# Performance work log

Hardware: AMD Instinct MI355X
Metric: run time of the kernel (lower is better)

The kernel has to match this reference:

```python
import jax, jax.numpy as jnp
import numpy as np

# dims matching init_kwargs
L = 2          # lstm_depth
H = 512        # lstm_size
E = 512        # text_embedding_size
V = 32000      # vocab_size
FH = 512       # feature_embedding_hidden_size
FEAT = 2048    # feature_size
START_IDX = 3.0  # start_of_seq_token_idx (used as a fill value, per original code)


def _lstm_cell(x, h, c, Wih, Whh, b):
    # PyTorch gate order: i, f, g, o. Wih:[in,4H], Whh:[H,4H], b:[4H]
    gates = x @ Wih + h @ Whh + b  # [B,4H]
    i, f, g, o = jnp.split(gates, 4, axis=-1)
    c_new = jax.nn.sigmoid(f) * c + jax.nn.sigmoid(i) * jnp.tanh(g)
    h_new = jax.nn.sigmoid(o) * jnp.tanh(c_new)
    return h_new, c_new


def setup_inputs() -> dict:
    key = jax.random.key(0)
    ks = jax.random.split(key, 12)
    B, N, T = 64, 49, 40
    s = 0.02
    img_data = jax.random.normal(ks[0], (B, N, FEAT), jnp.float32)
    W_fh = jax.random.normal(ks[1], (FEAT, FH), jnp.float32) * s
    b_fh = jnp.zeros((FH,), jnp.float32)
    Wc = jax.random.normal(ks[2], (L, FH, H), jnp.float32) * s
    bc = jnp.zeros((L, H), jnp.float32)
    Wh = jax.random.normal(ks[3], (L, FH, H), jnp.float32) * s
    bh = jnp.zeros((L, H), jnp.float32)
    W_ih = jax.random.normal(ks[4], (L, E, 4 * H), jnp.float32) * 0.04
    W_hh = jax.random.normal(ks[5], (L, H, 4 * H), jnp.float32) * 0.04
    b_lstm = jnp.zeros((L, 4 * H), jnp.float32)
    emb = jax.random.normal(ks[6], (V, E), jnp.float32) * s
    u = jax.random.uniform(ks[7], (T, B, V), jnp.float32, minval=1e-6, maxval=1.0 - 1e-6)
    gumbel = -jnp.log(-jnp.log(u))  # Gumbel(0,1) noise: Gumbel-max == Categorical.sample
    return {
        "img_data": img_data, "W_fh": W_fh, "b_fh": b_fh,
        "Wc": Wc, "bc": bc, "Wh": Wh, "bh": bh,
        "W_ih": W_ih, "W_hh": W_hh, "b_lstm": b_lstm,
        "emb": emb, "gumbel": gumbel, "max_seq_len": 40,
    }


def reference(img_data, W_fh, b_fh, Wc, bc, Wh, bh, W_ih, W_hh, b_lstm, emb, gumbel, max_seq_len):
    B = img_data.shape[0]
    # f_embedding = tanh(Linear(img_data)) : [B,N,FH]
    f_emb = jnp.tanh(img_data @ W_fh + b_fh)
    # mean over regions commutes with the per-layer Linear: mean(f @ W + b) = mean(f) @ W + b
    f_mean = jnp.mean(f_emb, axis=1)  # [B,FH]
    c0 = jnp.einsum('bf,lfh->lbh', f_mean, Wc) + bc[:, None, :]  # [L,B,H]
    h0 = jnp.einsum('bf,lfh->lbh', f_mean, Wh) + bh[:, None, :]
    # initial "embedding" is zeros + start_of_seq_token_idx (a constant fill, per original)
    x0 = jnp.full((B, E), START_IDX, dtype=img_data.dtype)
    emb_T = emb.T  # [E,V]

    def step(carry, g_t):
        h, c, x = carry  # h,c:[L,B,H], x:[B,E]; g_t:[B,V]
        inp = x
        hs, cs = [], []
        for l in range(L):  # small static depth
            hn, cn = _lstm_cell(inp, h[l], c[l], W_ih[l], W_hh[l], b_lstm[l])
            hs.append(hn); cs.append(cn)
            inp = hn
        logits = inp @ emb_T                      # [B,V]
        logp = jax.nn.log_softmax(logits, axis=-1)
        tok = jnp.argmax(logp + g_t, axis=-1)     # Gumbel-max categorical sample
        lp = jnp.take_along_axis(logp, tok[:, None], axis=1)[:, 0]  # [B]
        x_next = emb[tok]                         # next-step embedding lookup
        return (jnp.stack(hs, 0), jnp.stack(cs, 0), x_next), (tok, lp)

    _, (tokens, log_probs) = jax.lax.scan(step, (h0, c0, x0), gumbel)
    return tokens.T, log_probs.T  # [B,T], [B,T]
```

## Files before the change

kernel.cpp:

```cpp
#include <hip/hip_runtime.h>
#include <cmath>

namespace {

constexpr int BATCH = 64;
constexpr int NREG  = 49;
constexpr int FEATN = 2048;
constexpr int FHN   = 512;
constexpr int HID   = 512;
constexpr int EMBN  = 512;
constexpr int VOC   = 32000;
constexpr int TSTEPS= 40;
constexpr int G4    = 2048;
constexpr int NVT   = VOC / 128;

typedef short bf16x8 __attribute__((ext_vector_type(8)));
typedef float f32x4  __attribute__((ext_vector_type(4)));

__device__ __forceinline__ float sigm(float x) { return 1.0f / (1.0f + expf(-x)); }

__device__ __forceinline__ unsigned short f2bf(float f) {
  unsigned u = __float_as_uint(f);
  unsigned r = (u + 0x7fffu + ((u >> 16) & 1u)) >> 16;
  return (unsigned short)r;
}
__device__ __forceinline__ float bf2f(unsigned short h) {
  return __uint_as_float(((unsigned)h) << 16);
}

__device__ __forceinline__ bool better(float a, int ia, float b, int ib) {
  return a > b || (a == b && ia < ib);
}
__device__ __forceinline__ void top2_merge(float& v1, int& i1, float& v2, int& i2,
                                           float u1, int j1, float u2, int j2) {
  if (better(u1, j1, v1, i1)) {
    float t = v1; int ti = i1;
    v1 = u1; i1 = j1;
    if (better(u2, j2, t, ti)) { v2 = u2; i2 = j2; } else { v2 = t; i2 = ti; }
  } else {
    if (better(u1, j1, v2, i2)) { v2 = u1; i2 = j1; }
  }
}
__device__ __forceinline__ void lse_merge(float& m, float& s, float om, float os) {
  float nm = fmaxf(m, om);
  float ns = 0.f;
  if (m  > -INFINITY) ns += s  * expf(m  - nm);
  if (om > -INFINITY) ns += os * expf(om - nm);
  m = nm; s = ns;
}

__global__ __launch_bounds__(256) void k_trans(const float* __restrict__ src,
    unsigned short* __restrict__ dhi, unsigned short* __restrict__ dlo, int K, int N) {
  __shared__ float tile[32][33];
  const int k0 = blockIdx.x * 32, n0 = blockIdx.y * 32;
  const int tx = threadIdx.x & 31, ty = threadIdx.x >> 5;
#pragma unroll
  for (int r = ty; r < 32; r += 8) tile[r][tx] = src[(size_t)(k0 + r) * N + n0 + tx];
  __syncthreads();
#pragma unroll
  for (int r = ty; r < 32; r += 8) {
    float v = tile[tx][r];
    unsigned short hv = f2bf(v);
    size_t o = (size_t)(n0 + r) * K + k0 + tx;
    dhi[o] = hv;
    dlo[o] = f2bf(v - bf2f(hv));
  }
}

__global__ void k_split(const float* __restrict__ src, unsigned short* __restrict__ dhi,
                        unsigned short* __restrict__ dlo) {
  const size_t i = (size_t)blockIdx.x * 256 + threadIdx.x;
  const float4* p = reinterpret_cast<const float4*>(src) + i * 2;
  float4 a = p[0], b = p[1];
  float v[8] = {a.x, a.y, a.z, a.w, b.x, b.y, b.z, b.w};
  unsigned short hi[8], lo[8];
#pragma unroll
  for (int j = 0; j < 8; ++j) {
    hi[j] = f2bf(v[j]);
    lo[j] = f2bf(v[j] - bf2f(hi[j]));
  }
  uint4 oh, ol;
  oh.x = hi[0] | (hi[1] << 16); oh.y = hi[2] | (hi[3] << 16);
  oh.z = hi[4] | (hi[5] << 16); oh.w = hi[6] | (hi[7] << 16);
  ol.x = lo[0] | (lo[1] << 16); ol.y = lo[2] | (lo[3] << 16);
  ol.z = lo[4] | (lo[5] << 16); ol.w = lo[6] | (lo[7] << 16);
  reinterpret_cast<uint4*>(dhi)[i] = oh;
  reinterpret_cast<uint4*>(dlo)[i] = ol;
}

__global__ void k_emb2bf(const float* __restrict__ emb, unsigned short* __restrict__ ebf) {
  const size_t i = (size_t)blockIdx.x * 256 + threadIdx.x;
  const float4* p = reinterpret_cast<const float4*>(emb) + i * 2;
  float4 a = p[0], b = p[1];
  uint4 o;
  o.x = (unsigned)f2bf(a.x) | ((unsigned)f2bf(a.y) << 16);
  o.y = (unsigned)f2bf(a.z) | ((unsigned)f2bf(a.w) << 16);
  o.z = (unsigned)f2bf(b.x) | ((unsigned)f2bf(b.y) << 16);
  o.w = (unsigned)f2bf(b.z) | ((unsigned)f2bf(b.w) << 16);
  reinterpret_cast<uint4*>(ebf)[i] = o;
}

__global__ __launch_bounds__(256) void k_feat_mfma(
    const unsigned short* __restrict__ Ahi, const unsigned short* __restrict__ Alo,
    const unsigned short* __restrict__ Bhi, const unsigned short* __restrict__ Blo,
    const float* __restrict__ bias, float* __restrict__ femb) {
  const int m0 = blockIdx.x * 64, n0 = blockIdx.y * 64;
  const int tid = threadIdx.x, lane = tid & 63, w = tid >> 6;
  const int l15 = lane & 15, l4 = lane >> 4;
  f32x4 acc[4];
#pragma unroll
  for (int nt = 0; nt < 4; ++nt) acc[nt] = (f32x4){0.f, 0.f, 0.f, 0.f};
  const size_t arow = (size_t)(m0 + w * 16 + l15) * FEATN;
  for (int kk = 0; kk < FEATN / 32; ++kk) {
    const int k = kk * 32 + l4 * 8;
    bf16x8 a1 = *reinterpret_cast<const bf16x8*>(Ahi + arow + k);
    bf16x8 a2 = *reinterpret_cast<const bf16x8*>(Alo + arow + k);
#pragma unroll
    for (int nt = 0; nt < 4; ++nt) {
      const size_t brow = (size_t)(n0 + nt * 16 + l15) * FEATN + k;
      bf16x8 b1 = *reinterpret_cast<const bf16x8*>(Bhi + brow);
      bf16x8 b2 = *reinterpret_cast<const bf16x8*>(Blo + brow);
      acc[nt] = __builtin_amdgcn_mfma_f32_16x16x32_bf16(a1, b1, acc[nt], 0, 0, 0);
      acc[nt] = __builtin_amdgcn_mfma_f32_16x16x32_bf16(a1, b2, acc[nt], 0, 0, 0);
      acc[nt] = __builtin_amdgcn_mfma_f32_16x16x32_bf16(a2, b1, acc[nt], 0, 0, 0);
    }
  }
#pragma unroll
  for (int nt = 0; nt < 4; ++nt)
#pragma unroll
    for (int i = 0; i < 4; ++i) {
      int m = m0 + w * 16 + l4 * 4 + i, n = n0 + nt * 16 + l15;
      femb[(size_t)m * FHN + n] = tanhf(acc[nt][i] + bias[n]);
    }
}

__global__ void k_mean(const float* __restrict__ femb, float* __restrict__ fmean) {
  const int gid = blockIdx.x * 256 + threadIdx.x;
  const int b = gid >> 9, f = gid & 511;
  float s = 0.f;
  for (int n = 0; n < NREG; ++n) s += femb[(size_t)(b * NREG + n) * FHN + f];
  fmean[gid] = s * (1.0f / NREG);
}

__global__ __launch_bounds__(256) void k_h0c0(const float* __restrict__ fmean,
    const float* __restrict__ Wc, const float* __restrict__ bc,
    const float* __restrict__ Wh, const float* __restrict__ bh,
    float* __restrict__ hbuf, float* __restrict__ cbuf,
    unsigned short* __restrict__ hshi, unsigned short* __restrict__ hslo) {
  const int n0 = blockIdx.x * 64, l = blockIdx.y, isH = blockIdx.z;
  const float* W   = (isH ? Wh : Wc) + (size_t)l * FHN * HID;
  const float* bias= (isH ? bh : bc) + l * HID;
  float* outp      = (isH ? hbuf : cbuf) + (size_t)l * BATCH * HID;
  __shared__ float As[16][68], Bs[16][68];
  const int tid = threadIdx.x, tx = tid & 15, ty = tid >> 4;
  float acc[4][4] = {};
  for (int k0 = 0; k0 < FHN; k0 += 16) {
#pragma unroll
    for (int e = 0; e < 4; ++e) { int idx = tid + e * 256, m = idx >> 4, k = idx & 15; As[k][m] = fmean[m * FHN + k0 + k]; }
#pragma unroll
    for (int e = 0; e < 4; ++e) { int idx = tid + e * 256, k = idx >> 6, n = idx & 63; Bs[k][n] = W[(size_t)(k0 + k) * HID + n0 + n]; }
    __syncthreads();
#pragma unroll
    for (int k = 0; k < 16; ++k) {
      float4 av = *(const float4*)&As[k][ty * 4];
      float4 bv = *(const float4*)&Bs[k][tx * 4];
      float a[4] = {av.x, av.y, av.z, av.w}, b[4] = {bv.x, bv.y, bv.z, bv.w};
#pragma unroll
      for (int i = 0; i < 4; ++i)
#pragma unroll
        for (int j = 0; j < 4; ++j) acc[i][j] = fmaf(a[i], b[j], acc[i][j]);
    }
    __syncthreads();
  }
#pragma unroll
  for (int i = 0; i < 4; ++i) {
    int m = ty * 4 + i, n = n0 + tx * 4;
    float vals[4];
#pragma unroll
    for (int j = 0; j < 4; ++j) vals[j] = acc[i][j] + bias[n + j];
    *(float4*)&outp[(size_t)m * HID + n] = make_float4(vals[0], vals[1], vals[2], vals[3]);
    if (isH) {
#pragma unroll
      for (int j = 0; j < 4; ++j) {
        unsigned short hv = f2bf(vals[j]);
        size_t o = (size_t)l * BATCH * HID + (size_t)m * HID + n + j;
        hshi[o] = hv;
        hslo[o] = f2bf(vals[j] - bf2f(hv));
      }
    }
  }
}

__global__ void k_initx(unsigned short* __restrict__ xhi, unsigned short* __restrict__ xlo) {
  const int i = blockIdx.x * 256 + threadIdx.x;
  xhi[i] = 0x4040; xlo[i] = 0;
}

__global__ __launch_bounds__(256) void k_gates_mfma(
    const unsigned short* __restrict__ xhi, const unsigned short* __restrict__ xlo,
    const unsigned short* __restrict__ hhi, const unsigned short* __restrict__ hlo,
    const unsigned short* __restrict__ wih_hi, const unsigned short* __restrict__ wih_lo,
    const unsigned short* __restrict__ whh_hi, const unsigned short* __restrict__ whh_lo,
    float* __restrict__ part) {
  const int n0 = blockIdx.x * 64;
  const int ks = blockIdx.y;
  const unsigned short *Ah, *Al, *Wh_, *Wl;
  int kbase;
  if (ks < 4) { Ah = xhi; Al = xlo; Wh_ = wih_hi; Wl = wih_lo; kbase = ks * 128; }
  else        { Ah = hhi; Al = hlo; Wh_ = whh_hi; Wl = whh_lo; kbase = (ks - 4) * 128; }
  const int tid = threadIdx.x, lane = tid & 63, w = tid >> 6;
  const int l15 = lane & 15, l4 = lane >> 4;
  f32x4 acc[4];
#pragma unroll
  for (int nt = 0; nt < 4; ++nt) acc[nt] = (f32x4){0.f, 0.f, 0.f, 0.f};
  const size_t arow = (size_t)(w * 16 + l15) * EMBN;
#pragma unroll
  for (int kk = 0; kk < 4; ++kk) {
    const int k = kbase + kk * 32 + l4 * 8;
    bf16x8 a1 = *reinterpret_cast<const bf16x8*>(Ah + arow + k);
    bf16x8 a2 = *reinterpret_cast<const bf16x8*>(Al + arow + k);
#pragma unroll
    for (int nt = 0; nt < 4; ++nt) {
      const size_t brow = (size_t)(n0 + nt * 16 + l15) * EMBN + k;
      bf16x8 b1 = *reinterpret_cast<const bf16x8*>(Wh_ + brow);
      bf16x8 b2 = *reinterpret_cast<const bf16x8*>(Wl + brow);
      acc[nt] = __builtin_amdgcn_mfma_f32_16x16x32_bf16(a1, b1, acc[nt], 0, 0, 0);
      acc[nt] = __builtin_amdgcn_mfma_f32_16x16x32_bf16(a1, b2, acc[nt], 0, 0, 0);
      acc[nt] = __builtin_amdgcn_mfma_f32_16x16x32_bf16(a2, b1, acc[nt], 0, 0, 0);
    }
  }
  float* pp = part + (size_t)ks * BATCH * G4;
#pragma unroll
  for (int nt = 0; nt < 4; ++nt)
#pragma unroll
    for (int i = 0; i < 4; ++i) {
      int b = w * 16 + l4 * 4 + i, n = n0 + nt * 16 + l15;
      pp[(size_t)b * G4 + n] = acc[nt][i];
    }
}

__global__ void k_cell(const float* __restrict__ part, const float* __restrict__ bias,
                       float* __restrict__ h, float* __restrict__ c,
                       unsigned short* __restrict__ hhi, unsigned short* __restrict__ hlo) {
  const int gid = blockIdx.x * 256 + threadIdx.x;
  const int b = gid >> 9, j = gid & 511;
  float gi = bias[j], gf = bias[j + 512], gg = bias[j + 1024], go = bias[j + 1536];
#pragma unroll
  for (int ks = 0; ks < 8; ++ks) {
    const float* p = part + (size_t)ks * BATCH * G4 + (size_t)b * G4;
    gi += p[j]; gf += p[j + 512]; gg += p[j + 1024]; go += p[j + 1536];
  }
  float cn = sigm(gf) * c[gid] + sigm(gi) * tanhf(gg);
  float hn = sigm(go) * tanhf(cn);
  c[gid] = cn; h[gid] = hn;
  unsigned short hv = f2bf(hn);
  hhi[gid] = hv;
  hlo[gid] = f2bf(hn - bf2f(hv));
}

__global__ __launch_bounds__(256) void k_logits_mfma(
    const unsigned short* __restrict__ embbf,
    const unsigned short* __restrict__ h1bf,
    const float* __restrict__ gum,
    float* __restrict__ red) {
  const int v0 = blockIdx.x * 128;
  const int tid = threadIdx.x;
  const int lane = tid & 63, w = tid >> 6;
  const int l15 = lane & 15, l4 = lane >> 4;

  __shared__ unsigned short hl[32768];
  __shared__ float rm_[256], rs_[256], rv1_[256], rv2_[256];
  __shared__ int   ri1_[256], ri2_[256];

#pragma unroll
  for (int i = 0; i < 16; ++i) {
    int c = tid + i * 256;
    int row = c >> 6;
    int inb = (c & 63) << 4;
    uint4 v = *reinterpret_cast<const uint4*>(h1bf + ((size_t)c << 3));
    int sw = inb ^ ((row & 7) << 4);
    *reinterpret_cast<uint4*>(reinterpret_cast<char*>(hl) + row * 1024 + sw) = v;
  }
  __syncthreads();

  f32x4 acc[2][4];
#pragma unroll
  for (int m = 0; m < 2; ++m)
#pragma unroll
    for (int n = 0; n < 4; ++n) acc[m][n] = (f32x4){0.f, 0.f, 0.f, 0.f};

  const unsigned short* aptr = embbf + (size_t)(v0 + w * 32 + l15) * 512 + l4 * 8;
#pragma unroll
  for (int ks = 0; ks < 16; ++ks) {
    bf16x8 a0 = *reinterpret_cast<const bf16x8*>(aptr + ks * 32);
    bf16x8 a1 = *reinterpret_cast<const bf16x8*>(aptr + 16 * 512 + ks * 32);
    bf16x8 bb[4];
#pragma unroll
    for (int n = 0; n < 4; ++n) {
      int row = n * 16 + l15;
      int inb = ks * 64 + l4 * 16;
      int sw = inb ^ ((row & 7) << 4);
      bb[n] = *reinterpret_cast<const bf16x8*>(reinterpret_cast<const char*>(hl) + row * 1024 + sw);
    }
#pragma unroll
    for (int n = 0; n < 4; ++n) {
      acc[0][n] = __builtin_amdgcn_mfma_f32_16x16x32_bf16(a0, bb[n], acc[0][n], 0, 0, 0);
      acc[1][n] = __builtin_amdgcn_mfma_f32_16x16x32_bf16(a1, bb[n], acc[1][n], 0, 0, 0);
    }
  }

  const int vb = v0 + w * 32 + l4 * 4;
#pragma unroll
  for (int n = 0; n < 4; ++n) {
    const int b = n * 16 + l15;
    const float* gb = gum + (size_t)b * VOC + vb;
    float4 g0 = *reinterpret_cast<const float4*>(gb);
    float4 g1 = *reinterpret_cast<const float4*>(gb + 16);
    float lg[8] = {acc[0][n][0], acc[0][n][1], acc[0][n][2], acc[0][n][3],
                   acc[1][n][0], acc[1][n][1], acc[1][n][2], acc[1][n][3]};
    float gv[8] = {g0.x, g0.y, g0.z, g0.w, g1.x, g1.y, g1.z, g1.w};
    float mx = lg[0];
#pragma unroll
    for (int i = 1; i < 8; ++i) mx = fmaxf(mx, lg[i]);
    float ss = 0.f;
    float v1 = -INFINITY, v2 = -INFINITY; int i1 = 0x7fffffff, i2 = 0x7fffffff;
#pragma unroll
    for (int i = 0; i < 8; ++i) {
      ss += expf(lg[i] - mx);
      float val = lg[i] + gv[i];
      int idx = vb + (i & 3) + ((i >> 2) << 4);
      if (better(val, idx, v1, i1)) { v2 = v1; i2 = i1; v1 = val; i1 = idx; }
      else if (better(val, idx, v2, i2)) { v2 = val; i2 = idx; }
    }
#pragma unroll
    for (int mask = 16; mask <= 32; mask <<= 1) {
      float om = __shfl_xor(mx, mask);
      float os = __shfl_xor(ss, mask);
      float u1 = __shfl_xor(v1, mask); int j1 = __shfl_xor(i1, mask);
      float u2 = __shfl_xor(v2, mask); int j2 = __shfl_xor(i2, mask);
      lse_merge(mx, ss, om, os);
      top2_merge(v1, i1, v2, i2, u1, j1, u2, j2);
    }
    if (lane < 16) {
      int slot = (w * 4 + n) * 16 + l15;
      rm_[slot] = mx; rs_[slot] = ss;
      rv1_[slot] = v1; ri1_[slot] = i1; rv2_[slot] = v2; ri2_[slot] = i2;
    }
  }
  __syncthreads();
  if (tid < 64) {
    const int n = tid >> 4, c = tid & 15;
    int s0 = n * 16 + c;
    float M = rm_[s0], S = rs_[s0], V1 = rv1_[s0], V2 = rv2_[s0];
    int I1 = ri1_[s0], I2 = ri2_[s0];
#pragma unroll
    for (int ww = 1; ww < 4; ++ww) {
      int sl = (ww * 4 + n) * 16 + c;
      lse_merge(M, S, rm_[sl], rs_[sl]);
      top2_merge(V1, I1, V2, I2, rv1_[sl], ri1_[sl], rv2_[sl], ri2_[sl]);
    }
    float* rp = red + ((size_t)blockIdx.x * 64 + tid) * 8;
    rp[0] = M; rp[1] = S;
    rp[2] = V1; rp[3] = __int_as_float(I1);
    rp[4] = V2; rp[5] = __int_as_float(I2);
  }
}

__global__ __launch_bounds__(256) void k_sample(const float* __restrict__ red,
    const float* __restrict__ emb, const float* __restrict__ h1f, const float* __restrict__ gum,
    unsigned short* __restrict__ xhi, unsigned short* __restrict__ xlo,
    float* __restrict__ out, int t) {
  const int b = blockIdx.x, tid = threadIdx.x;
  __shared__ float rm[256], rs[256], rv1[256], rv2[256];
  __shared__ int   ri1[256], ri2[256];
  float m = -INFINITY, s = 0.f, v1 = -INFINITY, v2 = -INFINITY;
  int i1 = 0x7fffffff, i2 = 0x7fffffff;
  if (tid < NVT) {
    const float* rp = red + ((size_t)tid * 64 + b) * 8;
    m = rp[0]; s = rp[1];
    v1 = rp[2]; i1 = __float_as_int(rp[3]);
    v2 = rp[4]; i2 = __float_as_int(rp[5]);
  }
  rm[tid] = m; rs[tid] = s; rv1[tid] = v1; ri1[tid] = i1; rv2[tid] = v2; ri2[tid] = i2;
  __syncthreads();
  for (int off = 128; off > 0; off >>= 1) {
    if (tid < off) {
      float M = rm[tid], S = rs[tid];
      lse_merge(M, S, rm[tid + off], rs[tid + off]);
      rm[tid] = M; rs[tid] = S;
      float a1 = rv1[tid], a2 = rv2[tid]; int c1 = ri1[tid], c2 = ri2[tid];
      top2_merge(a1, c1, a2, c2, rv1[tid + off], ri1[tid + off], rv2[tid + off], ri2[tid + off]);
      rv1[tid] = a1; ri1[tid] = c1; rv2[tid] = a2; ri2[tid] = c2;
    }
    __syncthreads();
  }
  const int I1 = ri1[0], I2 = ri2[0];
  const float lse = rm[0] + logf(rs[0]);
  __shared__ float s1[256], s2[256];
  const float* e1 = emb + (size_t)I1 * EMBN;
  const float* e2 = emb + (size_t)I2 * EMBN;
  const float* hb = h1f + b * EMBN;
  float d1 = 0.f, d2 = 0.f;
  for (int k = tid; k < EMBN; k += 256) {
    float hv = hb[k];
    d1 = fmaf(e1[k], hv, d1);
    d2 = fmaf(e2[k], hv, d2);
  }
  s1[tid] = d1; s2[tid] = d2;
  __syncthreads();
  for (int off = 128; off > 0; off >>= 1) {
    if (tid < off) { s1[tid] += s1[tid + off]; s2[tid] += s2[tid + off]; }
    __syncthreads();
  }
  const float x1 = s1[0] + gum[(size_t)b * VOC + I1];
  const float x2 = s2[0] + gum[(size_t)b * VOC + I2];
  int tok; float dsel;
  if (x2 > x1 || (x2 == x1 && I2 < I1)) { tok = I2; dsel = s2[0]; }
  else                                  { tok = I1; dsel = s1[0]; }
  const float* et = emb + (size_t)tok * EMBN;
  for (int k = tid; k < EMBN; k += 256) {
    float ev = et[k];
    unsigned short hv = f2bf(ev);
    xhi[b * EMBN + k] = hv;
    xlo[b * EMBN + k] = f2bf(ev - bf2f(hv));
  }
  if (tid == 0) {
    out[b * TSTEPS + t] = (float)tok;
    out[BATCH * TSTEPS + b * TSTEPS + t] = dsel - lse;
  }
}

}

extern "C" void kernel_launch(void* const* d_in, const int* in_sizes, int n_in,
                              void* d_out, int out_size, void* d_ws, size_t ws_size,
                              hipStream_t stream) {
  const float* img  = (const float*)d_in[0];
  const float* W_fh = (const float*)d_in[1];
  const float* b_fh = (const float*)d_in[2];
  const float* Wc   = (const float*)d_in[3];
  const float* bc   = (const float*)d_in[4];
  const float* Wh   = (const float*)d_in[5];
  const float* bh   = (const float*)d_in[6];
  const float* W_ih = (const float*)d_in[7];
  const float* W_hh = (const float*)d_in[8];
  const float* b_l  = (const float*)d_in[9];
  const float* emb  = (const float*)d_in[10];
  const float* gum  = (const float*)d_in[11];
  float* out = (float*)d_out;

  float* w     = (float*)d_ws;
  float* femb  = w;
  float* fmean = femb + (size_t)3136 * 512;
  float* hbuf  = fmean + 64 * 512;
  float* cbuf  = hbuf + 2 * 64 * 512;
  float* part  = cbuf + 2 * 64 * 512;
  float* red   = part + (size_t)8 * 64 * 2048;

  unsigned short* us = (unsigned short*)(red + 250 * 64 * 8);
  unsigned short* embbf  = us;
  unsigned short* imghi  = embbf + (size_t)VOC * EMBN;
  unsigned short* imglo  = imghi + (size_t)3136 * 2048;
  unsigned short* wfh_hi = imglo + (size_t)3136 * 2048;
  unsigned short* wfh_lo = wfh_hi + (size_t)512 * 2048;
  unsigned short* wg     = wfh_lo + (size_t)512 * 2048;
  const size_t WGM = (size_t)2048 * 512;
  unsigned short* xhi    = wg + 8 * WGM;
  unsigned short* xlo    = xhi + 64 * 512;
  unsigned short* hshi   = xlo + 64 * 512;
  unsigned short* hslo   = hshi + 2 * 64 * 512;

  auto wgp = [&](int l, int mat, int part_) -> unsigned short* {
    return wg + (((size_t)l * 2 + mat) * 2 + part_) * WGM;
  };

  k_emb2bf<<<8000, 256, 0, stream>>>(emb, embbf);
  k_split<<<3136 * 2048 / 8 / 256, 256, 0, stream>>>(img, imghi, imglo);
  k_trans<<<dim3(FEATN / 32, FHN / 32), 256, 0, stream>>>(W_fh, wfh_hi, wfh_lo, FEATN, FHN);
  for (int l = 0; l < 2; ++l) {
    k_trans<<<dim3(EMBN / 32, G4 / 32), 256, 0, stream>>>(W_ih + (size_t)l * EMBN * G4, wgp(l, 0, 0), wgp(l, 0, 1), EMBN, G4);
    k_trans<<<dim3(HID / 32, G4 / 32), 256, 0, stream>>>(W_hh + (size_t)l * HID * G4, wgp(l, 1, 0), wgp(l, 1, 1), HID, G4);
  }
  k_feat_mfma<<<dim3(49, 8), 256, 0, stream>>>(imghi, imglo, wfh_hi, wfh_lo, b_fh, femb);
  k_mean<<<128, 256, 0, stream>>>(femb, fmean);
  k_h0c0<<<dim3(8, 2, 2), 256, 0, stream>>>(fmean, Wc, bc, Wh, bh, hbuf, cbuf, hshi, hslo);
  k_initx<<<128, 256, 0, stream>>>(xhi, xlo);

  for (int t = 0; t < TSTEPS; ++t) {
    const float* gum_t = gum + (size_t)t * BATCH * VOC;
    k_gates_mfma<<<dim3(32, 8), 256, 0, stream>>>(xhi, xlo, hshi, hslo,
        wgp(0, 0, 0), wgp(0, 0, 1), wgp(0, 1, 0), wgp(0, 1, 1), part);
    k_cell<<<128, 256, 0, stream>>>(part, b_l, hbuf, cbuf, hshi, hslo);
    k_gates_mfma<<<dim3(32, 8), 256, 0, stream>>>(hshi, hslo, hshi + 64 * 512, hslo + 64 * 512,
        wgp(1, 0, 0), wgp(1, 0, 1), wgp(1, 1, 0), wgp(1, 1, 1), part);
    k_cell<<<128, 256, 0, stream>>>(part, b_l + 2048, hbuf + 64 * 512, cbuf + 64 * 512,
                                    hshi + 64 * 512, hslo + 64 * 512);
    k_logits_mfma<<<NVT, 256, 0, stream>>>(embbf, hshi + 64 * 512, gum_t, red);
    k_sample<<<64, 256, 0, stream>>>(red, emb, hbuf + 64 * 512, gum_t, xhi, xlo, out, t);
  }
}
```

Measured before the change: 2.040 ms.

## Fuse LSTM gate GEMM and cell update into one kernel with ping-pong state

```diff
diff --git a/kernel.cpp b/kernel.cpp
--- a/kernel.cpp
+++ b/kernel.cpp
@@ -28,6 +28,13 @@
   return __uint_as_float(((unsigned)h) << 16);
 }
 
+__device__ __forceinline__ bf16x8 ntload_bf(const unsigned short* p) {
+  return __builtin_nontemporal_load(reinterpret_cast<const bf16x8*>(p));
+}
+__device__ __forceinline__ f32x4 ntload_f4(const float* p) {
+  return __builtin_nontemporal_load(reinterpret_cast<const f32x4*>(p));
+}
+
 __device__ __forceinline__ bool better(float a, int ia, float b, int ib) {
   return a > b || (a == b && ia < ib);
 }
@@ -48,6 +55,7 @@
   if (om > -INFINITY) ns += os * expf(om - nm);
   m = nm; s = ns;
 }
+
 
 __global__ __launch_bounds__(256) void k_trans(const float* __restrict__ src,
     unsigned short* __restrict__ dhi, unsigned short* __restrict__ dlo, int K, int N) {
@@ -196,69 +204,65 @@
   xhi[i] = 0x4040; xlo[i] = 0;
 }
 
-__global__ __launch_bounds__(256) void k_gates_mfma(
-    const unsigned short* __restrict__ xhi, const unsigned short* __restrict__ xlo,
-    const unsigned short* __restrict__ hhi, const unsigned short* __restrict__ hlo,
+
+__global__ __launch_bounds__(1024) void k_lstm(
+    const unsigned short* __restrict__ xh, const unsigned short* __restrict__ xl,
+    const unsigned short* __restrict__ hh, const unsigned short* __restrict__ hl,
     const unsigned short* __restrict__ wih_hi, const unsigned short* __restrict__ wih_lo,
     const unsigned short* __restrict__ whh_hi, const unsigned short* __restrict__ whh_lo,
-    float* __restrict__ part) {
-  const int n0 = blockIdx.x * 64;
-  const int ks = blockIdx.y;
-  const unsigned short *Ah, *Al, *Wh_, *Wl;
-  int kbase;
-  if (ks < 4) { Ah = xhi; Al = xlo; Wh_ = wih_hi; Wl = wih_lo; kbase = ks * 128; }
-  else        { Ah = hhi; Al = hlo; Wh_ = whh_hi; Wl = whh_lo; kbase = (ks - 4) * 128; }
-  const int tid = threadIdx.x, lane = tid & 63, w = tid >> 6;
+    const float* __restrict__ bias,
+    float* __restrict__ hbufl, float* __restrict__ cbufl,
+    unsigned short* __restrict__ ho_hi, unsigned short* __restrict__ ho_lo) {
+  __shared__ float gs[4][64][16];
+  const int bl = blockIdx.x, tid = threadIdx.x;
+  const int lane = tid & 63, w = tid >> 6;
   const int l15 = lane & 15, l4 = lane >> 4;
-  f32x4 acc[4];
-#pragma unroll
-  for (int nt = 0; nt < 4; ++nt) acc[nt] = (f32x4){0.f, 0.f, 0.f, 0.f};
-  const size_t arow = (size_t)(w * 16 + l15) * EMBN;
-#pragma unroll
-  for (int kk = 0; kk < 4; ++kk) {
-    const int k = kbase + kk * 32 + l4 * 8;
-    bf16x8 a1 = *reinterpret_cast<const bf16x8*>(Ah + arow + k);
-    bf16x8 a2 = *reinterpret_cast<const bf16x8*>(Al + arow + k);
-#pragma unroll
-    for (int nt = 0; nt < 4; ++nt) {
-      const size_t brow = (size_t)(n0 + nt * 16 + l15) * EMBN + k;
-      bf16x8 b1 = *reinterpret_cast<const bf16x8*>(Wh_ + brow);
-      bf16x8 b2 = *reinterpret_cast<const bf16x8*>(Wl + brow);
-      acc[nt] = __builtin_amdgcn_mfma_f32_16x16x32_bf16(a1, b1, acc[nt], 0, 0, 0);
-      acc[nt] = __builtin_amdgcn_mfma_f32_16x16x32_bf16(a1, b2, acc[nt], 0, 0, 0);
-      acc[nt] = __builtin_amdgcn_mfma_f32_16x16x32_bf16(a2, b1, acc[nt], 0, 0, 0);
-    }
-  }
-  float* pp = part + (size_t)ks * BATCH * G4;
-#pragma unroll
-  for (int nt = 0; nt < 4; ++nt)
-#pragma unroll
-    for (int i = 0; i < 4; ++i) {
-      int b = w * 16 + l4 * 4 + i, n = n0 + nt * 16 + l15;
-      pp[(size_t)b * G4 + n] = acc[nt][i];
-    }
-}
-
-__global__ void k_cell(const float* __restrict__ part, const float* __restrict__ bias,
-                       float* __restrict__ h, float* __restrict__ c,
-                       unsigned short* __restrict__ hhi, unsigned short* __restrict__ hlo) {
-  const int gid = blockIdx.x * 256 + threadIdx.x;
-  const int b = gid >> 9, j = gid & 511;
-  float gi = bias[j], gf = bias[j + 512], gg = bias[j + 1024], go = bias[j + 1536];
-#pragma unroll
-  for (int ks = 0; ks < 8; ++ks) {
-    const float* p = part + (size_t)ks * BATCH * G4 + (size_t)b * G4;
-    gi += p[j]; gf += p[j + 512]; gg += p[j + 1024]; go += p[j + 1536];
-  }
-  float cn = sigm(gf) * c[gid] + sigm(gi) * tanhf(gg);
-  float hn = sigm(go) * tanhf(cn);
-  c[gid] = cn; h[gid] = hn;
-  unsigned short hv = f2bf(hn);
-  hhi[gid] = hv;
-  hlo[gid] = f2bf(hn - bf2f(hv));
-}
-
-__global__ __launch_bounds__(256) void k_logits_mfma(
+  const int g = w >> 2, mt = w & 3;
+  const size_t nrow = (size_t)(g * 512 + bl * 16 + l15) * 512;
+  const size_t arow = (size_t)(mt * 16 + l15) * 512;
+  f32x4 acc = (f32x4){0.f, 0.f, 0.f, 0.f};
+#pragma unroll
+  for (int ks = 0; ks < 16; ++ks) {
+    const int k = ks * 32 + l4 * 8;
+    bf16x8 b1 = *reinterpret_cast<const bf16x8*>(wih_hi + nrow + k);
+    bf16x8 b2 = *reinterpret_cast<const bf16x8*>(wih_lo + nrow + k);
+    bf16x8 a1 = *reinterpret_cast<const bf16x8*>(xh + arow + k);
+    bf16x8 a2 = *reinterpret_cast<const bf16x8*>(xl + arow + k);
+    acc = __builtin_amdgcn_mfma_f32_16x16x32_bf16(a1, b1, acc, 0, 0, 0);
+    acc = __builtin_amdgcn_mfma_f32_16x16x32_bf16(a1, b2, acc, 0, 0, 0);
+    acc = __builtin_amdgcn_mfma_f32_16x16x32_bf16(a2, b1, acc, 0, 0, 0);
+  }
+#pragma unroll
+  for (int ks = 0; ks < 16; ++ks) {
+    const int k = ks * 32 + l4 * 8;
+    bf16x8 b1 = *reinterpret_cast<const bf16x8*>(whh_hi + nrow + k);
+    bf16x8 b2 = *reinterpret_cast<const bf16x8*>(whh_lo + nrow + k);
+    bf16x8 a1 = *reinterpret_cast<const bf16x8*>(hh + arow + k);
+    bf16x8 a2 = *reinterpret_cast<const bf16x8*>(hl + arow + k);
+    acc = __builtin_amdgcn_mfma_f32_16x16x32_bf16(a1, b1, acc, 0, 0, 0);
+    acc = __builtin_amdgcn_mfma_f32_16x16x32_bf16(a1, b2, acc, 0, 0, 0);
+    acc = __builtin_amdgcn_mfma_f32_16x16x32_bf16(a2, b1, acc, 0, 0, 0);
+  }
+#pragma unroll
+  for (int i = 0; i < 4; ++i)
+    gs[g][mt * 16 + l4 * 4 + i][l15] = acc[i];
+  __syncthreads();
+  {
+    const int b = tid >> 4, jl = tid & 15, j = bl * 16 + jl;
+    float gi = gs[0][b][jl] + bias[j];
+    float gf = gs[1][b][jl] + bias[512 + j];
+    float gg = gs[2][b][jl] + bias[1024 + j];
+    float go = gs[3][b][jl] + bias[1536 + j];
+    const size_t o = (size_t)b * HID + j;
+    float cn = sigm(gf) * cbufl[o] + sigm(gi) * tanhf(gg);
+    float hn = sigm(go) * tanhf(cn);
+    cbufl[o] = cn; hbufl[o] = hn;
+    unsigned short hv = f2bf(hn);
+    ho_hi[o] = hv; ho_lo[o] = f2bf(hn - bf2f(hv));
+  }
+}
+
+__global__ __launch_bounds__(256) void k_logits(
     const unsigned short* __restrict__ embbf,
     const unsigned short* __restrict__ h1bf,
     const float* __restrict__ gum,
@@ -292,8 +296,8 @@
   const unsigned short* aptr = embbf + (size_t)(v0 + w * 32 + l15) * 512 + l4 * 8;
 #pragma unroll
   for (int ks = 0; ks < 16; ++ks) {
-    bf16x8 a0 = *reinterpret_cast<const bf16x8*>(aptr + ks * 32);
-    bf16x8 a1 = *reinterpret_cast<const bf16x8*>(aptr + 16 * 512 + ks * 32);
+    bf16x8 a0 = ntload_bf(aptr + ks * 32);
+    bf16x8 a1 = ntload_bf(aptr + 16 * 512 + ks * 32);
     bf16x8 bb[4];
 #pragma unroll
     for (int n = 0; n < 4; ++n) {
@@ -314,11 +318,11 @@
   for (int n = 0; n < 4; ++n) {
     const int b = n * 16 + l15;
     const float* gb = gum + (size_t)b * VOC + vb;
-    float4 g0 = *reinterpret_cast<const float4*>(gb);
-    float4 g1 = *reinterpret_cast<const float4*>(gb + 16);
+    f32x4 g0 = ntload_f4(gb);
+    f32x4 g1 = ntload_f4(gb + 16);
     float lg[8] = {acc[0][n][0], acc[0][n][1], acc[0][n][2], acc[0][n][3],
                    acc[1][n][0], acc[1][n][1], acc[1][n][2], acc[1][n][3]};
-    float gv[8] = {g0.x, g0.y, g0.z, g0.w, g1.x, g1.y, g1.z, g1.w};
+    float gv[8] = {g0[0], g0[1], g0[2], g0[3], g1[0], g1[1], g1[2], g1[3]};
     float mx = lg[0];
 #pragma unroll
     for (int i = 1; i < 8; ++i) mx = fmaxf(mx, lg[i]);
@@ -454,8 +458,7 @@
   float* fmean = femb + (size_t)3136 * 512;
   float* hbuf  = fmean + 64 * 512;
   float* cbuf  = hbuf + 2 * 64 * 512;
-  float* part  = cbuf + 2 * 64 * 512;
-  float* red   = part + (size_t)8 * 64 * 2048;
+  float* red   = cbuf + 2 * 64 * 512;
 
   unsigned short* us = (unsigned short*)(red + 250 * 64 * 8);
   unsigned short* embbf  = us;
@@ -464,15 +467,18 @@
   unsigned short* wfh_hi = imglo + (size_t)3136 * 2048;
   unsigned short* wfh_lo = wfh_hi + (size_t)512 * 2048;
   unsigned short* wg     = wfh_lo + (size_t)512 * 2048;
-  const size_t WGM = (size_t)2048 * 512;
+  const size_t WGM = (size_t)G4 * 512;
   unsigned short* xhi    = wg + 8 * WGM;
   unsigned short* xlo    = xhi + 64 * 512;
   unsigned short* hshi   = xlo + 64 * 512;
-  unsigned short* hslo   = hshi + 2 * 64 * 512;
+  unsigned short* hslo   = hshi + (size_t)4 * 64 * 512;
 
   auto wgp = [&](int l, int mat, int part_) -> unsigned short* {
     return wg + (((size_t)l * 2 + mat) * 2 + part_) * WGM;
   };
+  const size_t HS = (size_t)BATCH * HID;
+  auto hs_hi = [&](int par, int l) { return hshi + ((size_t)par * 2 + l) * HS; };
+  auto hs_lo = [&](int par, int l) { return hslo + ((size_t)par * 2 + l) * HS; };
 
   k_emb2bf<<<8000, 256, 0, stream>>>(emb, embbf);
   k_split<<<3136 * 2048 / 8 / 256, 256, 0, stream>>>(img, imghi, imglo);
@@ -488,14 +494,14 @@
 
   for (int t = 0; t < TSTEPS; ++t) {
     const float* gum_t = gum + (size_t)t * BATCH * VOC;
-    k_gates_mfma<<<dim3(32, 8), 256, 0, stream>>>(xhi, xlo, hshi, hslo,
-        wgp(0, 0, 0), wgp(0, 0, 1), wgp(0, 1, 0), wgp(0, 1, 1), part);
-    k_cell<<<128, 256, 0, stream>>>(part, b_l, hbuf, cbuf, hshi, hslo);
-    k_gates_mfma<<<dim3(32, 8), 256, 0, stream>>>(hshi, hslo, hshi + 64 * 512, hslo + 64 * 512,
-        wgp(1, 0, 0), wgp(1, 0, 1), wgp(1, 1, 0), wgp(1, 1, 1), part);
-    k_cell<<<128, 256, 0, stream>>>(part, b_l + 2048, hbuf + 64 * 512, cbuf + 64 * 512,
-                                    hshi + 64 * 512, hslo + 64 * 512);
-    k_logits_mfma<<<NVT, 256, 0, stream>>>(embbf, hshi + 64 * 512, gum_t, red);
-    k_sample<<<64, 256, 0, stream>>>(red, emb, hbuf + 64 * 512, gum_t, xhi, xlo, out, t);
-  }
-}
+    const int p = t & 1, q = p ^ 1;
+    k_lstm<<<32, 1024, 0, stream>>>(xhi, xlo, hs_hi(p, 0), hs_lo(p, 0),
+        wgp(0, 0, 0), wgp(0, 0, 1), wgp(0, 1, 0), wgp(0, 1, 1),
+        b_l, hbuf, cbuf, hs_hi(q, 0), hs_lo(q, 0));
+    k_lstm<<<32, 1024, 0, stream>>>(hs_hi(q, 0), hs_lo(q, 0), hs_hi(p, 1), hs_lo(p, 1),
+        wgp(1, 0, 0), wgp(1, 0, 1), wgp(1, 1, 0), wgp(1, 1, 1),
+        b_l + 2048, hbuf + HS, cbuf + HS, hs_hi(q, 1), hs_lo(q, 1));
+    k_logits<<<NVT, 256, 0, stream>>>(embbf, hs_hi(q, 1), gum_t, red);
+    k_sample<<<64, 256, 0, stream>>>(red, emb, hbuf + HS, gum_t, xhi, xlo, out, t);
+  }
+}
```

Result: slower. 5.882 ms (+188.3%).
